# Performance work log

Measured on AMD Instinct MI355X. Metric: run time of the kernel, lower is better.

Reference implementation:

```python
import jax, jax.numpy as jnp
import numpy as np

B, S, HID, DK, DV, H = 4, 2048, 1024, 1024, 1024, 16
NEG = -1e9


def setup_inputs() -> dict:
    key = jax.random.key(0)
    ks = jax.random.split(key, 7)
    sc = HID ** -0.5
    queries = jax.random.normal(ks[0], (B, S, HID), jnp.float32)
    keys_ = jax.random.normal(ks[1], (B, S, HID), jnp.float32)
    values = jax.random.normal(ks[2], (B, S, HID), jnp.float32)
    Wq = jax.random.normal(ks[3], (HID, DK), jnp.float32) * sc
    Wk = jax.random.normal(ks[4], (HID, DK), jnp.float32) * sc
    Wv = jax.random.normal(ks[5], (HID, DV), jnp.float32) * sc
    Wo = jax.random.normal(ks[6], (DV, HID), jnp.float32) * sc
    # additive causal mask buffer [1,1,S,S]: -1e9 above diagonal
    mask = jnp.where(jnp.tril(jnp.ones((S, S), jnp.bool_)), 0.0, NEG).astype(jnp.float32)[None, None]
    return {"queries": queries, "keys": keys_, "values": values, "mask": mask,
            "Wq": Wq, "Wk": Wk, "Wv": Wv, "Wo": Wo}


def reference(queries, keys, values, mask, Wq, Wk, Wv, Wo):
    scale = (DK // H) ** -0.5
    q = jnp.einsum('bsd,de->bse', queries, Wq)
    k = jnp.einsum('bsd,de->bse', keys, Wk)
    v = jnp.einsum('bsd,de->bse', values, Wv)
    # split heads -> [B, H, S, head_dim]
    q = q.reshape(B, S, H, DK // H).transpose(0, 2, 1, 3) * scale
    k = k.reshape(B, S, H, DK // H).transpose(0, 2, 1, 3)
    v = v.reshape(B, S, H, DV // H).transpose(0, 2, 1, 3)
    logits = jnp.einsum('bhqd,bhkd->bhqk', q, k) + mask[:, :, :S, :S]
    weights = jax.nn.softmax(logits, axis=-1)  # dropout p=0 (eval)
    ctx = jnp.einsum('bhqk,bhkd->bhqd', weights, v)
    ctx = ctx.transpose(0, 2, 1, 3).reshape(B, S, DV)
    return jnp.einsum('bsd,de->bse', ctx, Wo)
```

## Files before the change

### kernel.cpp

```cpp
#include <hip/hip_runtime.h>

typedef __bf16 bf16_t;
typedef __bf16 bf16x4 __attribute__((ext_vector_type(4)));
typedef __bf16 bf16x8 __attribute__((ext_vector_type(8)));
typedef float f32x4 __attribute__((ext_vector_type(4)));
typedef float f32x4v __attribute__((ext_vector_type(4)));

#define GLOAD_LDS16(gptr, lptr) \
  __builtin_amdgcn_global_load_lds((const __attribute__((address_space(1))) void*)(gptr), \
                                   (__attribute__((address_space(3))) void*)(lptr), 16, 0, 0)


__global__ __launch_bounds__(256) void cast_x_kernel(
    const float* __restrict__ q, const float* __restrict__ k,
    const float* __restrict__ v, bf16_t* __restrict__ out) {
  const int z = blockIdx.y;
  const float* src = (z == 0) ? q : (z == 1) ? k : v;
  size_t i = ((size_t)blockIdx.x * 256 + threadIdx.x) * 4;
  f32x4v val = *(const f32x4v*)(src + i);
  bf16x4 o;
  o[0] = (bf16_t)val[0]; o[1] = (bf16_t)val[1];
  o[2] = (bf16_t)val[2]; o[3] = (bf16_t)val[3];
  *(bf16x4*)(out + (size_t)z * 8388608 + i) = o;
}

__global__ __launch_bounds__(256) void cast_w_kernel(
    const float* __restrict__ W0, const float* __restrict__ W1,
    const float* __restrict__ W2, const float* __restrict__ W3,
    bf16_t* __restrict__ Wt) {
  const int z = blockIdx.z;
  const float* W = (z == 0) ? W0 : (z == 1) ? W1 : (z == 2) ? W2 : W3;
  const float sc = (z == 0) ? 0.18033688011112042f : 1.0f;
  __shared__ float tile[64][65];
  const int n0 = blockIdx.x * 64, k0 = blockIdx.y * 64;
  const int t = threadIdx.x;
  const int r = t >> 4, c4 = (t & 15) * 4;
#pragma unroll
  for (int p = 0; p < 4; p++) {
    f32x4v v = *(const f32x4v*)&W[(size_t)(k0 + r + p * 16) * 1024 + n0 + c4];
    tile[r + p * 16][c4 + 0] = v[0]; tile[r + p * 16][c4 + 1] = v[1];
    tile[r + p * 16][c4 + 2] = v[2]; tile[r + p * 16][c4 + 3] = v[3];
  }
  __syncthreads();
  const int r2 = t >> 3, c2 = (t & 7) * 8;
  bf16_t* dst = Wt + (size_t)z * 1048576;
#pragma unroll
  for (int p = 0; p < 2; p++) {
    bf16x8 o;
#pragma unroll
    for (int i = 0; i < 8; i++) o[i] = (bf16_t)(tile[c2 + i][r2 + p * 32] * sc);
    *(bf16x8*)&dst[(size_t)(n0 + r2 + p * 32) * 1024 + k0 + c2] = o;
  }
}

template <int EPI>
__global__ __launch_bounds__(256) void gemm_bt(
    const bf16_t* __restrict__ Abase, const bf16_t* __restrict__ Wtbase,
    void* __restrict__ outp) {
  __shared__ bf16_t As[128 * 32];
  __shared__ bf16_t Bs[128 * 32];
  const int mt = blockIdx.x, nt = blockIdx.y, z = blockIdx.z;
  const int tid = threadIdx.x, wave = tid >> 6, lane = tid & 63;
  const bf16_t* A = Abase + (size_t)z * 8388608 + (size_t)mt * 128 * 1024;
  const bf16_t* Bt = Wtbase + (size_t)z * 1048576 + (size_t)nt * 128 * 1024;

  const int wm = wave >> 1, wn = wave & 1;
  const int frow = lane & 15, fk = (lane >> 4) * 8;
  const int srow = lane >> 2, scol = (lane & 3) * 8;

  f32x4 acc[4][4];
#pragma unroll
  for (int i = 0; i < 4; i++)
#pragma unroll
    for (int j = 0; j < 4; j++) acc[i][j] = (f32x4){0.f, 0.f, 0.f, 0.f};

  for (int k0 = 0; k0 < 1024; k0 += 32) {
#pragma unroll
    for (int r = 0; r < 2; r++) {
      const int c = wave * 2 + r;
      GLOAD_LDS16(A + (size_t)(c * 16 + srow) * 1024 + k0 + scol, &As[c * 512]);
      GLOAD_LDS16(Bt + (size_t)(c * 16 + srow) * 1024 + k0 + scol, &Bs[c * 512]);
    }
    __syncthreads();
    bf16x8 af[4], bfr[4];
#pragma unroll
    for (int i = 0; i < 4; i++)
      af[i] = *(const bf16x8*)&As[(wm * 64 + i * 16 + frow) * 32 + fk];
#pragma unroll
    for (int j = 0; j < 4; j++)
      bfr[j] = *(const bf16x8*)&Bs[(wn * 64 + j * 16 + frow) * 32 + fk];
#pragma unroll
    for (int i = 0; i < 4; i++)
#pragma unroll
      for (int j = 0; j < 4; j++)
        acc[i][j] = __builtin_amdgcn_mfma_f32_16x16x32_bf16(af[i], bfr[j],
                                                            acc[i][j], 0, 0, 0);
    __syncthreads();
  }

  const int rbase = mt * 128 + wm * 64;
  if constexpr (EPI == 0) {
    bf16_t* out = (bf16_t*)outp + (size_t)z * 8388608;
    const int h = nt * 2 + wn;
#pragma unroll
    for (int i = 0; i < 4; i++)
#pragma unroll
      for (int j = 0; j < 4; j++)
#pragma unroll
        for (int r = 0; r < 4; r++) {
          int row_g = rbase + i * 16 + (lane >> 4) * 4 + r;
          int b = row_g >> 11, s = row_g & 2047;
          int dd = j * 16 + frow;
          out[(((size_t)(b * 16 + h)) * 2048 + s) * 64 + dd] = (bf16_t)acc[i][j][r];
        }
  } else {
    float* out = (float*)outp;
#pragma unroll
    for (int i = 0; i < 4; i++)
#pragma unroll
      for (int j = 0; j < 4; j++)
#pragma unroll
        for (int r = 0; r < 4; r++) {
          int row_g = rbase + i * 16 + (lane >> 4) * 4 + r;
          int col_g = nt * 128 + wn * 64 + j * 16 + frow;
          out[(size_t)row_g * 1024 + col_g] = acc[i][j][r];
        }
  }
}

__global__ __launch_bounds__(256) void attn_fwd(const bf16_t* __restrict__ qkv,
                                                bf16_t* __restrict__ ctx) {
  const int bh = blockIdx.x;
  const int y = blockIdx.y;
  const int tt = y >> 2, jj = y & 3;
  const int qt = (tt & 1) ? ((tt >> 1) + 2 * jj) : (15 - (tt >> 1) - 2 * jj);
  const int b = bh >> 4, h = bh & 15;
  const size_t HS = (size_t)2048 * 64;
  const bf16_t* Qp = qkv + (size_t)bh * HS;
  const bf16_t* Kp = qkv + 8388608 + (size_t)bh * HS;
  const bf16_t* Vp = qkv + 16777216 + (size_t)bh * HS;

  __shared__ bf16_t Klds[64 * 72];
  __shared__ bf16_t VT[64 * 68];

  const int tid = threadIdx.x, wave = tid >> 6, lane = tid & 63;
  const int q15 = lane & 15, g = lane >> 4;
  const int qbase = qt * 128 + wave * 32;
  const int ldrow = tid >> 3, ldcol = (tid & 7) * 8;

  bf16x8 qf[2][2];
#pragma unroll
  for (int mf = 0; mf < 2; mf++)
#pragma unroll
    for (int kf = 0; kf < 2; kf++)
      qf[mf][kf] = *(const bf16x8*)&Qp[(size_t)(qbase + mf * 16 + q15) * 64 +
                                       kf * 32 + g * 8];

  float m[2] = {-1e30f, -1e30f}, l[2] = {0.f, 0.f};
  f32x4 of[2][4];
#pragma unroll
  for (int mf = 0; mf < 2; mf++)
#pragma unroll
    for (int nd = 0; nd < 4; nd++) of[mf][nd] = (f32x4){0.f, 0.f, 0.f, 0.f};

  const int nkv = qt * 2 + 2;
  const int qmax = qbase + 31;

  bf16x8 kreg[2], vreg[2];
#pragma unroll
  for (int p = 0; p < 2; p++) {
    int row = ldrow + p * 32;
    kreg[p] = *(const bf16x8*)&Kp[(size_t)row * 64 + ldcol];
    vreg[p] = *(const bf16x8*)&Vp[(size_t)row * 64 + ldcol];
  }

  for (int kv = 0; kv < nkv; ++kv) {
    const int kv0 = kv * 64;
    __syncthreads();
#pragma unroll
    for (int p = 0; p < 2; p++) {
      int row = ldrow + p * 32;
      *(bf16x8*)&Klds[row * 72 + ldcol] = kreg[p];
#pragma unroll
      for (int i = 0; i < 8; i++) VT[(ldcol + i) * 68 + row] = vreg[p][i];
    }
    __syncthreads();

    if (kv + 1 < nkv) {
      const int kv1 = kv0 + 64;
#pragma unroll
      for (int p = 0; p < 2; p++) {
        int row = ldrow + p * 32;
        kreg[p] = *(const bf16x8*)&Kp[(size_t)(kv1 + row) * 64 + ldcol];
        vreg[p] = *(const bf16x8*)&Vp[(size_t)(kv1 + row) * 64 + ldcol];
      }
    }

    if (kv0 > qmax) continue;

    f32x4 sf[2][4];
    __builtin_amdgcn_s_setprio(1);
#pragma unroll
    for (int nf = 0; nf < 4; nf++) {
      bf16x8 ka = *(const bf16x8*)&Klds[(nf * 16 + q15) * 72 + g * 8];
      bf16x8 kb = *(const bf16x8*)&Klds[(nf * 16 + q15) * 72 + 32 + g * 8];
#pragma unroll
      for (int mf = 0; mf < 2; mf++) {
        f32x4 a = (f32x4){0.f, 0.f, 0.f, 0.f};
        a = __builtin_amdgcn_mfma_f32_16x16x32_bf16(ka, qf[mf][0], a, 0, 0, 0);
        a = __builtin_amdgcn_mfma_f32_16x16x32_bf16(kb, qf[mf][1], a, 0, 0, 0);
        sf[mf][nf] = a;
      }
    }
    __builtin_amdgcn_s_setprio(0);

    if (kv >= 2 * qt + (wave >> 1)) {
#pragma unroll
      for (int mf = 0; mf < 2; mf++) {
        int q_g = qbase + mf * 16 + q15;
#pragma unroll
        for (int nf = 0; nf < 4; nf++)
#pragma unroll
          for (int r = 0; r < 4; r++)
            if (kv0 + nf * 16 + g * 4 + r > q_g) sf[mf][nf][r] = -1e30f;
      }
    }

    bf16x8 ap[2][2];
#pragma unroll
    for (int mf = 0; mf < 2; mf++) {
      float pmax = sf[mf][0][0];
#pragma unroll
      for (int nf = 0; nf < 4; nf++)
#pragma unroll
        for (int r = 0; r < 4; r++) pmax = fmaxf(pmax, sf[mf][nf][r]);
      pmax = fmaxf(pmax, __shfl_xor(pmax, 16));
      pmax = fmaxf(pmax, __shfl_xor(pmax, 32));
      float mold = m[mf];
      if (!__all(pmax <= mold + 8.0f)) {
        float mnew = fmaxf(mold, pmax);
        float alpha = __builtin_amdgcn_exp2f(mold - mnew);
        m[mf] = mnew;
        l[mf] *= alpha;
#pragma unroll
        for (int r = 0; r < 4; r++) {
          float aO = __shfl(alpha, (lane & 48) | (g * 4 + r));
#pragma unroll
          for (int nd = 0; nd < 4; nd++) of[mf][nd][r] *= aO;
        }
      }
      float mm = m[mf];
      float rs = 0.f;
#pragma unroll
      for (int nf = 0; nf < 4; nf++)
#pragma unroll
        for (int r = 0; r < 4; r++) {
          float pp = __builtin_amdgcn_exp2f(sf[mf][nf][r] - mm);
          sf[mf][nf][r] = pp;
          rs += pp;
        }
      rs += __shfl_xor(rs, 16);
      rs += __shfl_xor(rs, 32);
      l[mf] += rs;
#pragma unroll
      for (int kf = 0; kf < 2; kf++)
#pragma unroll
        for (int j2 = 0; j2 < 4; j2++) {
          ap[mf][kf][j2] = (bf16_t)sf[mf][2 * kf][j2];
          ap[mf][kf][j2 + 4] = (bf16_t)sf[mf][2 * kf + 1][j2];
        }
    }

    __builtin_amdgcn_s_setprio(1);
#pragma unroll
    for (int nd = 0; nd < 4; nd++) {
      const int d = nd * 16 + q15;
#pragma unroll
      for (int kf = 0; kf < 2; kf++) {
        bf16x4 v0 = *(const bf16x4*)&VT[d * 68 + kf * 32 + 4 * g];
        bf16x4 v1 = *(const bf16x4*)&VT[d * 68 + kf * 32 + 16 + 4 * g];
        bf16x8 vv;
#pragma unroll
        for (int i = 0; i < 4; i++) { vv[i] = v0[i]; vv[i + 4] = v1[i]; }
#pragma unroll
        for (int mf = 0; mf < 2; mf++)
          of[mf][nd] = __builtin_amdgcn_mfma_f32_16x16x32_bf16(ap[mf][kf], vv,
                                                               of[mf][nd], 0, 0, 0);
      }
    }
    __builtin_amdgcn_s_setprio(0);
  }

#pragma unroll
  for (int mf = 0; mf < 2; mf++) {
    float rcpO[4];
#pragma unroll
    for (int r = 0; r < 4; r++) {
      float lO = __shfl(l[mf], (lane & 48) | (g * 4 + r));
      rcpO[r] = 1.0f / lO;
    }
#pragma unroll
    for (int nd = 0; nd < 4; nd++)
#pragma unroll
      for (int r = 0; r < 4; r++) {
        int srow_ = qbase + mf * 16 + g * 4 + r;
        ctx[((size_t)(b * 2048 + srow_)) * 1024 + h * 64 + nd * 16 + q15] =
            (bf16_t)(of[mf][nd][r] * rcpO[r]);
      }
  }
}


extern "C" void kernel_launch(void* const* d_in, const int* in_sizes, int n_in,
                              void* d_out, int out_size, void* d_ws, size_t ws_size,
                              hipStream_t stream) {
  const float* queries = (const float*)d_in[0];
  const float* keys    = (const float*)d_in[1];
  const float* values  = (const float*)d_in[2];
  const float* Wq = (const float*)d_in[4];
  const float* Wk = (const float*)d_in[5];
  const float* Wv = (const float*)d_in[6];
  const float* Wo = (const float*)d_in[7];

  char* ws = (char*)d_ws;
  bf16_t* Xb  = (bf16_t*)ws;
  bf16_t* qkv = (bf16_t*)(ws + 50331648);
  bf16_t* Wt  = (bf16_t*)(ws + 100663296);
  bf16_t* ctx = Xb;
  float* out = (float*)d_out;

  cast_x_kernel<<<dim3(8192, 3), 256, 0, stream>>>(queries, keys, values, Xb);
  cast_w_kernel<<<dim3(16, 16, 4), 256, 0, stream>>>(Wq, Wk, Wv, Wo, Wt);
  gemm_bt<0><<<dim3(64, 8, 3), 256, 0, stream>>>(Xb, Wt, (void*)qkv);
  attn_fwd<<<dim3(64, 16), 256, 0, stream>>>(qkv, ctx);
  gemm_bt<1><<<dim3(64, 8, 1), 256, 0, stream>>>(ctx, Wt + 3 * 1048576, (void*)out);
}
```

Measured before the change: 206.5 us.

## Pair causal query tiles per block and double-buffer K/V in LDS

Each attention block now processes two query tiles (qt and 15-qt) sequentially, so every block gets the same causal workload, and the grid shrinks from 16 to 8 in y. K/V tiles are double-buffered in LDS, which lets the next tile be written while the current one is consumed, with one barrier per iteration instead of two. The transposed V store gets an XOR swizzle to reduce LDS bank conflicts, and the s_setprio hints are removed. The trade-off is half as many blocks in flight and twice the LDS per block.

After: 196.0 us. 1.05x faster.

```diff
diff --git a/kernel.cpp b/kernel.cpp
--- a/kernel.cpp
+++ b/kernel.cpp
@@ -132,181 +132,197 @@
                                                 bf16_t* __restrict__ ctx) {
   const int bh = blockIdx.x;
   const int y = blockIdx.y;
-  const int tt = y >> 2, jj = y & 3;
-  const int qt = (tt & 1) ? ((tt >> 1) + 2 * jj) : (15 - (tt >> 1) - 2 * jj);
   const int b = bh >> 4, h = bh & 15;
   const size_t HS = (size_t)2048 * 64;
   const bf16_t* Qp = qkv + (size_t)bh * HS;
   const bf16_t* Kp = qkv + 8388608 + (size_t)bh * HS;
   const bf16_t* Vp = qkv + 16777216 + (size_t)bh * HS;
 
-  __shared__ bf16_t Klds[64 * 72];
-  __shared__ bf16_t VT[64 * 68];
+  __shared__ bf16_t Klds[2][64 * 72];
+  __shared__ bf16_t VT[2][64 * 68];
 
   const int tid = threadIdx.x, wave = tid >> 6, lane = tid & 63;
   const int q15 = lane & 15, g = lane >> 4;
-  const int qbase = qt * 128 + wave * 32;
   const int ldrow = tid >> 3, ldcol = (tid & 7) * 8;
 
-  bf16x8 qf[2][2];
-#pragma unroll
-  for (int mf = 0; mf < 2; mf++)
-#pragma unroll
-    for (int kf = 0; kf < 2; kf++)
-      qf[mf][kf] = *(const bf16x8*)&Qp[(size_t)(qbase + mf * 16 + q15) * 64 +
-                                       kf * 32 + g * 8];
-
-  float m[2] = {-1e30f, -1e30f}, l[2] = {0.f, 0.f};
-  f32x4 of[2][4];
-#pragma unroll
-  for (int mf = 0; mf < 2; mf++)
-#pragma unroll
-    for (int nd = 0; nd < 4; nd++) of[mf][nd] = (f32x4){0.f, 0.f, 0.f, 0.f};
-
-  const int nkv = qt * 2 + 2;
-  const int qmax = qbase + 31;
-
-  bf16x8 kreg[2], vreg[2];
-#pragma unroll
-  for (int p = 0; p < 2; p++) {
-    int row = ldrow + p * 32;
-    kreg[p] = *(const bf16x8*)&Kp[(size_t)row * 64 + ldcol];
-    vreg[p] = *(const bf16x8*)&Vp[(size_t)row * 64 + ldcol];
-  }
-
-  for (int kv = 0; kv < nkv; ++kv) {
-    const int kv0 = kv * 64;
-    __syncthreads();
-#pragma unroll
-    for (int p = 0; p < 2; p++) {
-      int row = ldrow + p * 32;
-      *(bf16x8*)&Klds[row * 72 + ldcol] = kreg[p];
-#pragma unroll
-      for (int i = 0; i < 8; i++) VT[(ldcol + i) * 68 + row] = vreg[p][i];
+#pragma unroll 1
+  for (int s = 0; s < 2; s++) {
+    const int qt = s ? (15 - y) : y;
+    const int qbase = qt * 128 + wave * 32;
+    const int nkv = qt * 2 + 2;
+    const int qmax = qbase + 31;
+
+    bf16x8 qf[2][2];
+#pragma unroll
+    for (int mf = 0; mf < 2; mf++)
+#pragma unroll
+      for (int kf = 0; kf < 2; kf++)
+        qf[mf][kf] = *(const bf16x8*)&Qp[(size_t)(qbase + mf * 16 + q15) * 64 +
+                                         kf * 32 + g * 8];
+
+    float m[2] = {-1e30f, -1e30f}, l[2] = {0.f, 0.f};
+    f32x4 of[2][4];
+#pragma unroll
+    for (int mf = 0; mf < 2; mf++)
+#pragma unroll
+      for (int nd = 0; nd < 4; nd++) of[mf][nd] = (f32x4){0.f, 0.f, 0.f, 0.f};
+
+    {
+      bf16x8 kreg[2], vreg[2];
+#pragma unroll
+      for (int p = 0; p < 2; p++) {
+        int row = ldrow + p * 32;
+        kreg[p] = *(const bf16x8*)&Kp[(size_t)row * 64 + ldcol];
+        vreg[p] = *(const bf16x8*)&Vp[(size_t)row * 64 + ldcol];
+      }
+#pragma unroll
+      for (int p = 0; p < 2; p++) {
+        int row = ldrow + p * 32;
+        *(bf16x8*)&Klds[0][row * 72 + ldcol] = kreg[p];
+#pragma unroll
+        for (int i = 0; i < 8; i++)
+          VT[0][(ldcol + i) * 68 + (row ^ (ldcol & 56))] = vreg[p][i];
+      }
     }
     __syncthreads();
 
-    if (kv + 1 < nkv) {
-      const int kv1 = kv0 + 64;
-#pragma unroll
-      for (int p = 0; p < 2; p++) {
-        int row = ldrow + p * 32;
-        kreg[p] = *(const bf16x8*)&Kp[(size_t)(kv1 + row) * 64 + ldcol];
-        vreg[p] = *(const bf16x8*)&Vp[(size_t)(kv1 + row) * 64 + ldcol];
-      }
+    for (int kv = 0; kv < nkv; ++kv) {
+      const int kv0 = kv * 64;
+      const int cur = kv & 1;
+
+      bf16x8 kreg[2], vreg[2];
+      const bool havenext = (kv + 1 < nkv);
+      if (havenext) {
+        const int kv1 = kv0 + 64;
+#pragma unroll
+        for (int p = 0; p < 2; p++) {
+          int row = ldrow + p * 32;
+          kreg[p] = *(const bf16x8*)&Kp[(size_t)(kv1 + row) * 64 + ldcol];
+          vreg[p] = *(const bf16x8*)&Vp[(size_t)(kv1 + row) * 64 + ldcol];
+        }
+      }
+
+      if (kv0 <= qmax) {
+        f32x4 sf[2][4];
+#pragma unroll
+        for (int nf = 0; nf < 4; nf++) {
+          bf16x8 ka = *(const bf16x8*)&Klds[cur][(nf * 16 + q15) * 72 + g * 8];
+          bf16x8 kb = *(const bf16x8*)&Klds[cur][(nf * 16 + q15) * 72 + 32 + g * 8];
+#pragma unroll
+          for (int mf = 0; mf < 2; mf++) {
+            f32x4 a = (f32x4){0.f, 0.f, 0.f, 0.f};
+            a = __builtin_amdgcn_mfma_f32_16x16x32_bf16(ka, qf[mf][0], a, 0, 0, 0);
+            a = __builtin_amdgcn_mfma_f32_16x16x32_bf16(kb, qf[mf][1], a, 0, 0, 0);
+            sf[mf][nf] = a;
+          }
+        }
+
+        if (kv >= 2 * qt + (wave >> 1)) {
+#pragma unroll
+          for (int mf = 0; mf < 2; mf++) {
+            int q_g = qbase + mf * 16 + q15;
+#pragma unroll
+            for (int nf = 0; nf < 4; nf++)
+#pragma unroll
+              for (int r = 0; r < 4; r++)
+                if (kv0 + nf * 16 + g * 4 + r > q_g) sf[mf][nf][r] = -1e30f;
+          }
+        }
+
+        bf16x8 ap[2][2];
+#pragma unroll
+        for (int mf = 0; mf < 2; mf++) {
+          float pmax = sf[mf][0][0];
+#pragma unroll
+          for (int nf = 0; nf < 4; nf++)
+#pragma unroll
+            for (int r = 0; r < 4; r++) pmax = fmaxf(pmax, sf[mf][nf][r]);
+          pmax = fmaxf(pmax, __shfl_xor(pmax, 16));
+          pmax = fmaxf(pmax, __shfl_xor(pmax, 32));
+          float mold = m[mf];
+          if (!__all(pmax <= mold + 8.0f)) {
+            float mnew = fmaxf(mold, pmax);
+            float alpha = __builtin_amdgcn_exp2f(mold - mnew);
+            m[mf] = mnew;
+            l[mf] *= alpha;
+#pragma unroll
+            for (int r = 0; r < 4; r++) {
+              float aO = __shfl(alpha, (lane & 48) | (g * 4 + r));
+#pragma unroll
+              for (int nd = 0; nd < 4; nd++) of[mf][nd][r] *= aO;
+            }
+          }
+          float mm = m[mf];
+          float rs = 0.f;
+#pragma unroll
+          for (int nf = 0; nf < 4; nf++)
+#pragma unroll
+            for (int r = 0; r < 4; r++) {
+              float pp = __builtin_amdgcn_exp2f(sf[mf][nf][r] - mm);
+              sf[mf][nf][r] = pp;
+              rs += pp;
+            }
+          rs += __shfl_xor(rs, 16);
+          rs += __shfl_xor(rs, 32);
+          l[mf] += rs;
+#pragma unroll
+          for (int kf = 0; kf < 2; kf++)
+#pragma unroll
+            for (int j2 = 0; j2 < 4; j2++) {
+              ap[mf][kf][j2] = (bf16_t)sf[mf][2 * kf][j2];
+              ap[mf][kf][j2 + 4] = (bf16_t)sf[mf][2 * kf + 1][j2];
+            }
+        }
+
+#pragma unroll
+        for (int nd = 0; nd < 4; nd++) {
+          const int d = nd * 16 + q15;
+          const int swz8 = (d >> 3 & 7) * 8;
+#pragma unroll
+          for (int kf = 0; kf < 2; kf++) {
+            bf16x4 v0 = *(const bf16x4*)&VT[cur][d * 68 + ((kf * 32 + 4 * g) ^ swz8)];
+            bf16x4 v1 = *(const bf16x4*)&VT[cur][d * 68 + ((kf * 32 + 16 + 4 * g) ^ swz8)];
+            bf16x8 vv;
+#pragma unroll
+            for (int i = 0; i < 4; i++) { vv[i] = v0[i]; vv[i + 4] = v1[i]; }
+#pragma unroll
+            for (int mf = 0; mf < 2; mf++)
+              of[mf][nd] = __builtin_amdgcn_mfma_f32_16x16x32_bf16(ap[mf][kf], vv,
+                                                                   of[mf][nd], 0, 0, 0);
+          }
+        }
+      }
+
+      if (havenext) {
+#pragma unroll
+        for (int p = 0; p < 2; p++) {
+          int row = ldrow + p * 32;
+          *(bf16x8*)&Klds[cur ^ 1][row * 72 + ldcol] = kreg[p];
+#pragma unroll
+          for (int i = 0; i < 8; i++)
+            VT[cur ^ 1][(ldcol + i) * 68 + (row ^ (ldcol & 56))] = vreg[p][i];
+        }
+      }
+      __syncthreads();
     }
 
-    if (kv0 > qmax) continue;
-
-    f32x4 sf[2][4];
-    __builtin_amdgcn_s_setprio(1);
-#pragma unroll
-    for (int nf = 0; nf < 4; nf++) {
-      bf16x8 ka = *(const bf16x8*)&Klds[(nf * 16 + q15) * 72 + g * 8];
-      bf16x8 kb = *(const bf16x8*)&Klds[(nf * 16 + q15) * 72 + 32 + g * 8];
-#pragma unroll
-      for (int mf = 0; mf < 2; mf++) {
-        f32x4 a = (f32x4){0.f, 0.f, 0.f, 0.f};
-        a = __builtin_amdgcn_mfma_f32_16x16x32_bf16(ka, qf[mf][0], a, 0, 0, 0);
-        a = __builtin_amdgcn_mfma_f32_16x16x32_bf16(kb, qf[mf][1], a, 0, 0, 0);
-        sf[mf][nf] = a;
-      }
+#pragma unroll
+    for (int mf = 0; mf < 2; mf++) {
+      float rcpO[4];
+#pragma unroll
+      for (int r = 0; r < 4; r++) {
+        float lO = __shfl(l[mf], (lane & 48) | (g * 4 + r));
+        rcpO[r] = 1.0f / lO;
+      }
+#pragma unroll
+      for (int nd = 0; nd < 4; nd++)
+#pragma unroll
+        for (int r = 0; r < 4; r++) {
+          int srow_ = qbase + mf * 16 + g * 4 + r;
+          ctx[((size_t)(b * 2048 + srow_)) * 1024 + h * 64 + nd * 16 + q15] =
+              (bf16_t)(of[mf][nd][r] * rcpO[r]);
+        }
     }
-    __builtin_amdgcn_s_setprio(0);
-
-    if (kv >= 2 * qt + (wave >> 1)) {
-#pragma unroll
-      for (int mf = 0; mf < 2; mf++) {
-        int q_g = qbase + mf * 16 + q15;
-#pragma unroll
-        for (int nf = 0; nf < 4; nf++)
-#pragma unroll
-          for (int r = 0; r < 4; r++)
-            if (kv0 + nf * 16 + g * 4 + r > q_g) sf[mf][nf][r] = -1e30f;
-      }
-    }
-
-    bf16x8 ap[2][2];
-#pragma unroll
-    for (int mf = 0; mf < 2; mf++) {
-      float pmax = sf[mf][0][0];
-#pragma unroll
-      for (int nf = 0; nf < 4; nf++)
-#pragma unroll
-        for (int r = 0; r < 4; r++) pmax = fmaxf(pmax, sf[mf][nf][r]);
-      pmax = fmaxf(pmax, __shfl_xor(pmax, 16));
-      pmax = fmaxf(pmax, __shfl_xor(pmax, 32));
-      float mold = m[mf];
-      if (!__all(pmax <= mold + 8.0f)) {
-        float mnew = fmaxf(mold, pmax);
-        float alpha = __builtin_amdgcn_exp2f(mold - mnew);
-        m[mf] = mnew;
-        l[mf] *= alpha;
-#pragma unroll
-        for (int r = 0; r < 4; r++) {
-          float aO = __shfl(alpha, (lane & 48) | (g * 4 + r));
-#pragma unroll
-          for (int nd = 0; nd < 4; nd++) of[mf][nd][r] *= aO;
-        }
-      }
-      float mm = m[mf];
-      float rs = 0.f;
-#pragma unroll
-      for (int nf = 0; nf < 4; nf++)
-#pragma unroll
-        for (int r = 0; r < 4; r++) {
-          float pp = __builtin_amdgcn_exp2f(sf[mf][nf][r] - mm);
-          sf[mf][nf][r] = pp;
-          rs += pp;
-        }
-      rs += __shfl_xor(rs, 16);
-      rs += __shfl_xor(rs, 32);
-      l[mf] += rs;
-#pragma unroll
-      for (int kf = 0; kf < 2; kf++)
-#pragma unroll
-        for (int j2 = 0; j2 < 4; j2++) {
-          ap[mf][kf][j2] = (bf16_t)sf[mf][2 * kf][j2];
-          ap[mf][kf][j2 + 4] = (bf16_t)sf[mf][2 * kf + 1][j2];
-        }
-    }
-
-    __builtin_amdgcn_s_setprio(1);
-#pragma unroll
-    for (int nd = 0; nd < 4; nd++) {
-      const int d = nd * 16 + q15;
-#pragma unroll
-      for (int kf = 0; kf < 2; kf++) {
-        bf16x4 v0 = *(const bf16x4*)&VT[d * 68 + kf * 32 + 4 * g];
-        bf16x4 v1 = *(const bf16x4*)&VT[d * 68 + kf * 32 + 16 + 4 * g];
-        bf16x8 vv;
-#pragma unroll
-        for (int i = 0; i < 4; i++) { vv[i] = v0[i]; vv[i + 4] = v1[i]; }
-#pragma unroll
-        for (int mf = 0; mf < 2; mf++)
-          of[mf][nd] = __builtin_amdgcn_mfma_f32_16x16x32_bf16(ap[mf][kf], vv,
-                                                               of[mf][nd], 0, 0, 0);
-      }
-    }
-    __builtin_amdgcn_s_setprio(0);
-  }
-
-#pragma unroll
-  for (int mf = 0; mf < 2; mf++) {
-    float rcpO[4];
-#pragma unroll
-    for (int r = 0; r < 4; r++) {
-      float lO = __shfl(l[mf], (lane & 48) | (g * 4 + r));
-      rcpO[r] = 1.0f / lO;
-    }
-#pragma unroll
-    for (int nd = 0; nd < 4; nd++)
-#pragma unroll
-      for (int r = 0; r < 4; r++) {
-        int srow_ = qbase + mf * 16 + g * 4 + r;
-        ctx[((size_t)(b * 2048 + srow_)) * 1024 + h * 64 + nd * 16 + q15] =
-            (bf16_t)(of[mf][nd][r] * rcpO[r]);
-      }
   }
 }
 
@@ -332,6 +348,6 @@
   cast_x_kernel<<<dim3(8192, 3), 256, 0, stream>>>(queries, keys, values, Xb);
   cast_w_kernel<<<dim3(16, 16, 4), 256, 0, stream>>>(Wq, Wk, Wv, Wo, Wt);
   gemm_bt<0><<<dim3(64, 8, 3), 256, 0, stream>>>(Xb, Wt, (void*)qkv);
-  attn_fwd<<<dim3(64, 16), 256, 0, stream>>>(qkv, ctx);
+  attn_fwd<<<dim3(64, 8), 256, 0, stream>>>(qkv, ctx);
   gemm_bt<1><<<dim3(64, 8, 1), 256, 0, stream>>>(ctx, Wt + 3 * 1048576, (void*)out);
 }
```
